# Optimization experiments

Hardware: AMD Instinct MI355X
Metric: run time of the kernel (lower is better)

## Reference

```python
import jax, jax.numpy as jnp
import numpy as np

BLOCK_SIZE = 128  # config.block_size; first query block skips intra-block causal mask (faithful to source)
NEG = -1e9       # the module uses -1e9, not -inf, for masking and m_i init


def setup_inputs() -> dict:
    key = jax.random.key(0)
    kq, kk, kv, km = jax.random.split(key, 4)
    B, S, H, D = 2, 2048, 16, 64
    q = jax.random.normal(kq, (B, S, H, D), dtype=jnp.float32)
    k = jax.random.normal(kk, (B, S, H, D), dtype=jnp.float32)
    v = jax.random.normal(kv, (B, S, H, D), dtype=jnp.float32)
    mask = jax.random.randint(km, (B, S), 0, 2).astype(bool)
    mask = mask.at[:, 0].set(True)  # keep first key attendable
    return {"q": q, "k": k, "v": v, "mask": mask}


def reference(q, k, v, mask):
    # q,k,v: [B,S,H,D]; mask: [B,S] bool (True = attend)
    B, S, H, D = q.shape
    scale = 1.0 / np.sqrt(D)
    # config.normalize_query=True -> F.normalize(q, dim=-1) (eps=1e-12)
    qn = q / jnp.maximum(jnp.linalg.norm(q, axis=-1, keepdims=True), 1e-12)
    # scores: [B,S(query),H,S(key)]
    scores = jnp.einsum('bshd,bkhd->bshk', qn, k) * scale
    qi = jnp.arange(S)[:, None]
    ki = jnp.arange(S)[None, :]
    # Faithful causal structure of the blocked PyTorch fallback:
    #  - keys limited to k <= q (triu(diagonal=block_start+1) masking)
    #  - EXCEPT the first query block (block_start==0), where the intra-block
    #    causal mask is skipped (keys still limited to the first block).
    allowed = (ki <= qi) | ((qi < BLOCK_SIZE) & (ki < BLOCK_SIZE))  # [S,S]
    scores = jnp.where(allowed[None, :, None, :], scores, NEG)
    scores = jnp.where(mask[:, None, None, :], scores, NEG)
    p = jax.nn.softmax(scores, axis=-1)
    out = jnp.einsum('bshk,bkhd->bshd', p, v)
    return out
```

## Files before the change

kernel.cpp:

```cpp
#include <hip/hip_runtime.h>
#include <stdint.h>

typedef __attribute__((ext_vector_type(8))) short short8;
typedef __attribute__((ext_vector_type(4))) float floatx4;
typedef __attribute__((ext_vector_type(4))) unsigned int uintx4;
typedef __attribute__((ext_vector_type(2))) unsigned int uintx2;
typedef unsigned long long ulong64;

#define S_LEN 2048
#define NHEAD 16
#define DHEAD 64
#define KB    64
#define KPL   131072
#define VPL   262144
#define VOFF  (32 * KPL)
#define MOFF  (VOFF + 32 * VPL)
#define POFF  (MOFF + 8192)
#define DOFF  (POFF + 512 * 32768)
#define WS_NEEDED ((size_t)DOFF + 512 * 512)
#define NEGINF (-__builtin_inff())
#define CSC   0.011271055f

static __device__ __forceinline__ unsigned f2bf(float f) {
    union { float f; unsigned u; } w; w.f = f;
    return (w.u + 0x7FFFu + ((w.u >> 16) & 1u)) >> 16;
}
static __device__ __forceinline__ unsigned cvtpk(float lo, float hi) {
    unsigned r;
    asm("v_cvt_pk_bf16_f32 %0, %1, %2" : "=v"(r) : "v"(lo), "v"(hi));
    return r;
}
template <int HI>
static __device__ __forceinline__ int cvtfp8(float a, float b, int old) {
    return __builtin_amdgcn_cvt_pk_fp8_f32(a, b, old, HI);
}
static __device__ __forceinline__ floatx4 mfma16(short8 a, short8 b, floatx4 c) {
    return __builtin_amdgcn_mfma_f32_16x16x32_bf16(a, b, c, 0, 0, 0);
}
static __device__ __forceinline__ floatx4 mfma8(long a, long b, floatx4 c) {
    return __builtin_amdgcn_mfma_f32_16x16x32_fp8_fp8(a, b, c, 0, 0, 0);
}

__global__ __launch_bounds__(256) void prep_kernel(
    const float* __restrict__ kg, const float* __restrict__ vg,
    const int* __restrict__ mg, char* __restrict__ ws)
{
    __shared__ unsigned short Tl[64 * 72];
    const int bid = blockIdx.x;
    const int t   = bid & 31;
    const int bh  = bid >> 5;
    const int b   = bh >> 4, h = bh & 15;
    const int tid = threadIdx.x;
    char* kpre = ws + (size_t)bh * KPL;
    char* vpre = ws + VOFF + (size_t)bh * VPL;

    #pragma unroll
    for (int r2 = 0; r2 < 2; ++r2) {
        const int ss  = tid + r2 * 256;
        const int khs = ss >> 8;
        const int mt  = (ss >> 7) & 1;
        const int ksd = (ss >> 6) & 1;
        const int ln  = ss & 63;
        const int key = khs * 32 + mt * 16 + (ln & 15);
        const int d0  = 32 * ksd + 8 * (ln >> 4);
        const float* kr = kg + (((size_t)b * S_LEN + t * 64 + key) * NHEAD + h) * DHEAD + d0;
        floatx4 f0 = *(const floatx4*)(kr);
        floatx4 f1 = *(const floatx4*)(kr + 4);
        int w0 = 0, w1 = 0;
        w0 = cvtfp8<0>(f0[0], f0[1], w0); w0 = cvtfp8<1>(f0[2], f0[3], w0);
        w1 = cvtfp8<0>(f1[0], f1[1], w1); w1 = cvtfp8<1>(f1[2], f1[3], w1);
        *(uintx2*)(kpre + t * 4096 + ss * 8) = (uintx2){(unsigned)w0, (unsigned)w1};
    }
    {
        const int key = tid >> 2;
        const int d0  = (tid & 3) * 16;
        const float vz = mg[(size_t)b * S_LEN + t * 64 + key] ? 1.f : 0.f;
        const size_t grow = (((size_t)b * S_LEN + t * 64 + key) * NHEAD + h) * DHEAD;
        #pragma unroll
        for (int q = 0; q < 4; ++q) {
            floatx4 f = *(const floatx4*)(vg + grow + d0 + 4 * q);
            #pragma unroll
            for (int ii = 0; ii < 4; ++ii)
                Tl[(d0 + 4 * q + ii) * 72 + key] = (unsigned short)f2bf(f[ii] * vz);
        }
    }
    __syncthreads();
    #pragma unroll
    for (int r2 = 0; r2 < 2; ++r2) {
        const int ss  = tid + r2 * 256;
        const int khs = ss >> 8;
        const int nt  = (ss >> 6) & 3;
        const int ln  = ss & 63;
        const int d   = 16 * nt + (ln & 15);
        const int pg  = 4 * khs + (ln >> 4);
        unsigned short vals[8];
        #pragma unroll
        for (int i = 0; i < 8; ++i) {
            const int p   = pg * 8 + i;
            const int blk = p >> 5;
            const int a   = (p >> 3) & 3;
            const int key = 32 * blk + ((i < 4) ? (4 * a + i) : (16 + 4 * a + i - 4));
            vals[i] = Tl[d * 72 + key];
        }
        *(uintx4*)(vpre + t * 8192 + ss * 16) = *(const uintx4*)vals;
    }
    if (h == 0 && tid < 64) {
        const int key = tid;
        const int gg = (key >> 2) & 3, lo = key & 3;
        const int ks = key >> 5,      hi = (key >> 4) & 1;
        const unsigned short mv = mg[(size_t)b * S_LEN + t * 64 + key] ? 0x3F80 : 0;
        *(unsigned short*)(ws + MOFF + (size_t)b * 4096 + t * 128
                           + gg * 32 + ks * 16 + (4 * hi + lo) * 2) = mv;
    }
}

__global__ __launch_bounds__(512, 4) void fa3_main(
    const float* __restrict__ qg, char* __restrict__ ws,
    float* __restrict__ og)
{
    __shared__ char smem[32768];
    char* Qs = smem;

    const int tid  = threadIdx.x;
    const int bid  = blockIdx.x;
    const int gidx = bid >> 5;
    const int bh   = bid & 31;
    int qb, chunk; bool split;
    if (gidx < 16) { qb = 15 - (gidx >> 1); chunk = gidx & 1; split = true; }
    else           { qb = 7 - (gidx - 16);  chunk = 0;        split = false; }
    const int b    = bh >> 4;
    const int h    = bh & 15;
    const int w    = tid >> 6;
    const int lane = tid & 63;
    const int g    = lane >> 4;
    const int lm   = lane & 15;
    const int kh   = w >> 2;
    const int wq   = w & 3;
    const int nkt = (qb == 0) ? 2 : (2 * qb + 2);
    int kt0 = 0, kt1 = nkt;
    if (split) { const int hh = nkt >> 1; kt0 = chunk ? hh : 0; kt1 = chunk ? nkt : hh; }

    {
        const int r  = tid >> 2;
        const int q0 = tid & 3;
        const float* src = qg + (((size_t)b * S_LEN + (size_t)qb * 128 + r) * NHEAD + h) * DHEAD + q0 * 16;
        floatx4 f0 = *(const floatx4*)(src + 0);
        floatx4 f1 = *(const floatx4*)(src + 4);
        floatx4 f2 = *(const floatx4*)(src + 8);
        floatx4 f3 = *(const floatx4*)(src + 12);
        float ssq = 0.f;
        #pragma unroll
        for (int i = 0; i < 4; ++i)
            ssq += f0[i]*f0[i] + f1[i]*f1[i] + f2[i]*f2[i] + f3[i]*f3[i];
        ssq += __shfl_xor(ssq, 1);
        ssq += __shfl_xor(ssq, 2);
        const float sc = 16.0f / fmaxf(sqrtf(ssq), 1e-12f);
        int w0 = 0, w1 = 0, w2 = 0, w3 = 0;
        w0 = cvtfp8<0>(f0[0]*sc, f0[1]*sc, w0); w0 = cvtfp8<1>(f0[2]*sc, f0[3]*sc, w0);
        w1 = cvtfp8<0>(f1[0]*sc, f1[1]*sc, w1); w1 = cvtfp8<1>(f1[2]*sc, f1[3]*sc, w1);
        w2 = cvtfp8<0>(f2[0]*sc, f2[1]*sc, w2); w2 = cvtfp8<1>(f2[2]*sc, f2[3]*sc, w2);
        w3 = cvtfp8<0>(f3[0]*sc, f3[1]*sc, w3); w3 = cvtfp8<1>(f3[2]*sc, f3[3]*sc, w3);
        const int Xr = r & 7;
        char* qp = Qs + r * 64 + 8 * (((2 * q0) ^ Xr) & ~1);
        *(uintx4*)qp = (Xr & 1)
            ? (uintx4){(unsigned)w2, (unsigned)w3, (unsigned)w0, (unsigned)w1}
            : (uintx4){(unsigned)w0, (unsigned)w1, (unsigned)w2, (unsigned)w3};
    }
    __syncthreads();

    const int Xl8 = (lm & 7) << 3;
    long qf8[2][2];
    #pragma unroll
    for (int grp = 0; grp < 2; ++grp) {
        const char* base = Qs + (wq * 32 + grp * 16 + lm) * 64;
        #pragma unroll
        for (int ksd = 0; ksd < 2; ++ksd)
            qf8[grp][ksd] = *(const long*)(base + ((32 * ksd + 8 * g) ^ Xl8));
    }

    const char* kp = ws + (size_t)bh * KPL + (size_t)kt0 * 4096 + kh * 2048 + lane * 8;
    const char* vp = ws + VOFF + (size_t)bh * VPL + (size_t)kt0 * 8192 + kh * 4096 + lane * 16;
    const char* mp = ws + MOFF + (size_t)b * 4096 + (size_t)kt0 * 128 + g * 32 + kh * 16;

    floatx4 oacc[2][4];
    floatx4 dacc[2];
    #pragma unroll
    for (int grp = 0; grp < 2; ++grp) {
        dacc[grp] = (floatx4){0.f,0.f,0.f,0.f};
        #pragma unroll
        for (int nt = 0; nt < 4; ++nt) oacc[grp][nt] = (floatx4){0.f,0.f,0.f,0.f};
    }
    floatx4 ZERO4 = (floatx4){0.f,0.f,0.f,0.f};
    asm volatile("" : "+v"(ZERO4));
    const int qgl0 = qb * 128 + wq * 32 + lm;

    for (int kt = kt0; kt < kt1; ++kt) {
        const ulong64 k00 = *(const ulong64*)(kp);
        const ulong64 k01 = *(const ulong64*)(kp + 512);
        const ulong64 k10 = *(const ulong64*)(kp + 1024);
        const ulong64 k11 = *(const ulong64*)(kp + 1536);
        const short8 vf0 = *(const short8*)(vp);
        const short8 vf1 = *(const short8*)(vp + 1024);
        const short8 vf2 = *(const short8*)(vp + 2048);
        const short8 vf3 = *(const short8*)(vp + 3072);
        const short8 mf  = *(const short8*)(mp);
        kp += 4096; vp += 8192; mp += 128;

        floatx4 st[2][2];
        __builtin_amdgcn_s_setprio(1);
        st[0][0] = mfma8((long)k00, qf8[0][0], ZERO4);
        st[1][0] = mfma8((long)k00, qf8[1][0], ZERO4);
        st[0][1] = mfma8((long)k10, qf8[0][0], ZERO4);
        st[1][1] = mfma8((long)k10, qf8[1][0], ZERO4);
        st[0][0] = mfma8((long)k01, qf8[0][1], st[0][0]);
        st[1][0] = mfma8((long)k01, qf8[1][1], st[1][0]);
        st[0][1] = mfma8((long)k11, qf8[0][1], st[0][1]);
        st[1][1] = mfma8((long)k11, qf8[1][1], st[1][1]);
        __builtin_amdgcn_s_setprio(0);

        if ((qb >= 1) && (kt >= 2 * qb)) {
            #pragma unroll
            for (int mt = 0; mt < 2; ++mt)
                #pragma unroll
                for (int j = 0; j < 4; ++j) {
                    const int kgl = kt * KB + kh * 32 + mt * 16 + 4 * g + j;
                    if (kgl > qgl0)      st[0][mt][j] = -1e6f;
                    if (kgl > qgl0 + 16) st[1][mt][j] = -1e6f;
                }
        }

        short8 pa[2];
        #pragma unroll
        for (int grp = 0; grp < 2; ++grp) {
            float p[8];
            #pragma unroll
            for (int mt = 0; mt < 2; ++mt)
                #pragma unroll
                for (int j = 0; j < 4; ++j)
                    p[mt * 4 + j] = exp2f(fmaf(st[grp][mt][j], CSC, -8.0f));
            union { short8 s; uintx4 u; } pu;
            pu.u = (uintx4){ cvtpk(p[0], p[1]), cvtpk(p[2], p[3]),
                             cvtpk(p[4], p[5]), cvtpk(p[6], p[7]) };
            pa[grp] = pu.s;
        }
        __builtin_amdgcn_s_setprio(1);
        dacc[0] = mfma16(pa[0], mf, dacc[0]);
        dacc[1] = mfma16(pa[1], mf, dacc[1]);
        oacc[0][0] = mfma16(pa[0], vf0, oacc[0][0]);
        oacc[1][0] = mfma16(pa[1], vf0, oacc[1][0]);
        oacc[0][1] = mfma16(pa[0], vf1, oacc[0][1]);
        oacc[1][1] = mfma16(pa[1], vf1, oacc[1][1]);
        oacc[0][2] = mfma16(pa[0], vf2, oacc[0][2]);
        oacc[1][2] = mfma16(pa[1], vf2, oacc[1][2]);
        oacc[0][3] = mfma16(pa[0], vf3, oacc[0][3]);
        oacc[1][3] = mfma16(pa[1], vf3, oacc[1][3]);
        __builtin_amdgcn_s_setprio(0);
    }
    __syncthreads();

    floatx4* rbuf = (floatx4*)smem;
    float*   dbuf = (float*)smem;
    if (kh == 1) {
        #pragma unroll
        for (int grp = 0; grp < 2; ++grp)
            #pragma unroll
            for (int nt = 0; nt < 4; ++nt)
                rbuf[((grp * 4 + nt) * 4 + wq) * 64 + lane] = oacc[grp][nt];
    }
    __syncthreads();
    if (kh == 0) {
        #pragma unroll
        for (int grp = 0; grp < 2; ++grp)
            #pragma unroll
            for (int nt = 0; nt < 4; ++nt)
                oacc[grp][nt] += rbuf[((grp * 4 + nt) * 4 + wq) * 64 + lane];
    }
    __syncthreads();
    if (kh == 1 && lm == 0) {
        #pragma unroll
        for (int grp = 0; grp < 2; ++grp)
            #pragma unroll
            for (int j = 0; j < 4; ++j)
                dbuf[wq * 32 + grp * 16 + 4 * g + j] = dacc[grp][j];
    }
    __syncthreads();
    if (kh == 0) {
        if (!split) {
            #pragma unroll
            for (int grp = 0; grp < 2; ++grp)
                #pragma unroll
                for (int j = 0; j < 4; ++j) {
                    const int rl = wq * 32 + grp * 16 + 4 * g + j;
                    const float invj = 1.0f / (dacc[grp][j] + dbuf[rl]);
                    float* dst = og + (((size_t)b * S_LEN + qb * 128 + rl) * NHEAD + h) * DHEAD + lm;
                    #pragma unroll
                    for (int nt = 0; nt < 4; ++nt) dst[nt * 16] = oacc[grp][nt][j] * invj;
                }
        } else {
            const int s = ((qb - 8) * 32 + bh) * 2 + chunk;
            float* po = (float*)(ws + POFF + (size_t)s * 32768);
            float* pd = (float*)(ws + DOFF + (size_t)s * 512);
            #pragma unroll
            for (int grp = 0; grp < 2; ++grp)
                #pragma unroll
                for (int j = 0; j < 4; ++j) {
                    const int rl = wq * 32 + grp * 16 + 4 * g + j;
                    #pragma unroll
                    for (int nt = 0; nt < 4; ++nt)
                        po[rl * 64 + nt * 16 + lm] = oacc[grp][nt][j];
                    if (lm == 0) pd[rl] = dacc[grp][j] + dbuf[rl];
                }
        }
    }
}

__global__ __launch_bounds__(256) void fa3_combine(
    const char* __restrict__ ws, float* __restrict__ og)
{
    const int i0  = (blockIdx.x * 256 + threadIdx.x) * 8;
    const int d   = i0 & 63;
    const int row = (i0 >> 6) & 127;
    const int bh  = (i0 >> 13) & 31;
    const int qbi = i0 >> 18;
    const int b   = bh >> 4, h = bh & 15;
    const int s0  = (qbi * 32 + bh) * 2;
    const float* p0 = (const float*)(ws + POFF + (size_t)s0 * 32768) + row * 64 + d;
    const float* p1 = (const float*)(ws + POFF + (size_t)(s0 + 1) * 32768) + row * 64 + d;
    const float den = ((const float*)(ws + DOFF + (size_t)s0 * 512))[row]
                    + ((const float*)(ws + DOFF + (size_t)(s0 + 1) * 512))[row];
    const float inv = 1.0f / den;
    floatx4 a0 = *(const floatx4*)p0, a1 = *(const floatx4*)(p0 + 4);
    floatx4 b0 = *(const floatx4*)p1, b1 = *(const floatx4*)(p1 + 4);
    floatx4 o0, o1;
    #pragma unroll
    for (int i = 0; i < 4; ++i) { o0[i] = (a0[i] + b0[i]) * inv; o1[i] = (a1[i] + b1[i]) * inv; }
    float* dst = og + (((size_t)b * S_LEN + (8 + qbi) * 128 + row) * NHEAD + h) * DHEAD + d;
    *(floatx4*)dst       = o0;
    *(floatx4*)(dst + 4) = o1;
}

__global__ __launch_bounds__(512) void fa3_fallback(
    const float* __restrict__ qg, const float* __restrict__ kg,
    const float* __restrict__ vg, const int* __restrict__ mg,
    float* __restrict__ og)
{
    __shared__ unsigned short Qs[128 * DHEAD];
    __shared__ unsigned short Ks2[KB * DHEAD];
    __shared__ unsigned short Vt[DHEAD * KB];
    __shared__ float Ms[KB];

    const int tid  = threadIdx.x;
    const int bid  = blockIdx.x;
    const int qb   = 15 - (bid >> 5);
    const int bh   = bid & 31;
    const int b    = bh >> 4;
    const int h    = bh & 15;
    const int w    = tid >> 6;
    const int lane = tid & 63;
    const int g    = lane >> 4;
    const int lm   = lane & 15;

    {
        const int r  = tid >> 2;
        const int q0 = tid & 3;
        const float* src = qg + (((size_t)b * S_LEN + (size_t)qb * 128 + r) * NHEAD + h) * DHEAD + q0 * 16;
        floatx4 f0 = *(const floatx4*)(src + 0);
        floatx4 f1 = *(const floatx4*)(src + 4);
        floatx4 f2 = *(const floatx4*)(src + 8);
        floatx4 f3 = *(const floatx4*)(src + 12);
        float ssq = 0.f;
        #pragma unroll
        for (int i = 0; i < 4; ++i)
            ssq += f0[i]*f0[i] + f1[i]*f1[i] + f2[i]*f2[i] + f3[i]*f3[i];
        ssq += __shfl_xor(ssq, 1);
        ssq += __shfl_xor(ssq, 2);
        const float sc = 0.125f / fmaxf(sqrtf(ssq), 1e-12f);
        float fv[16];
        #pragma unroll
        for (int i = 0; i < 4; ++i) { fv[i]=f0[i]; fv[4+i]=f1[i]; fv[8+i]=f2[i]; fv[12+i]=f3[i]; }
        unsigned pk[8];
        #pragma unroll
        for (int i = 0; i < 8; ++i)
            pk[i] = f2bf(fv[2*i]*sc) | (f2bf(fv[2*i+1]*sc) << 16);
        const int X = (r & 7) << 4;
        char* qp = (char*)Qs + r * 128;
        *(uintx4*)(qp + ((32*q0)      ^ X)) = (uintx4){pk[0],pk[1],pk[2],pk[3]};
        *(uintx4*)(qp + ((32*q0 + 16) ^ X)) = (uintx4){pk[4],pk[5],pk[6],pk[7]};
    }
    __syncthreads();

    short8 qf[2];
    {
        const int row = w * 16 + lm;
        const int X = (row & 7) << 4;
        const char* base = (const char*)Qs + row * 128;
        #pragma unroll
        for (int ks = 0; ks < 2; ++ks) {
            union { short8 s; uintx2 u[2]; } u;
            u.u[0] = *(const uintx2*)(base + ((64*ks + 8*g)      ^ X));
            u.u[1] = *(const uintx2*)(base + ((64*ks + 8*g + 32) ^ X));
            qf[ks] = u.s;
        }
    }

    floatx4 oacc[4];
    #pragma unroll
    for (int nt = 0; nt < 4; ++nt) oacc[nt] = (floatx4){0.f,0.f,0.f,0.f};
    float mrun = NEGINF, lrun = 0.f;
    const int q_glob = qb * 128 + w * 16 + lm;
    const int nkt = (qb == 0) ? 2 : (2 * qb + 2);

    for (int kt = 0; kt < nkt; ++kt) {
        const int kb0 = kt * KB;
        {
            const int r = tid >> 3;
            const int o = tid & 7;
            const size_t goff = (((size_t)b * S_LEN + kb0 + r) * NHEAD + h) * DHEAD + o * 8;
            floatx4 a0 = *(const floatx4*)(kg + goff);
            floatx4 a1 = *(const floatx4*)(kg + goff + 4);
            floatx4 c0 = *(const floatx4*)(vg + goff);
            floatx4 c1 = *(const floatx4*)(vg + goff + 4);
            uintx4 kw = (uintx4){ f2bf(a0[0]) | (f2bf(a0[1])<<16),
                                  f2bf(a0[2]) | (f2bf(a0[3])<<16),
                                  f2bf(a1[0]) | (f2bf(a1[1])<<16),
                                  f2bf(a1[2]) | (f2bf(a1[3])<<16) };
            *(uintx4*)((char*)Ks2 + r*128 + ((16*o) ^ ((r & 7) << 4))) = kw;
            float cv[8];
            #pragma unroll
            for (int i = 0; i < 4; ++i) { cv[i] = c0[i]; cv[4+i] = c1[i]; }
            #pragma unroll
            for (int i = 0; i < 8; ++i) {
                const int d = 8*o + i;
                Vt[d*64 + (r ^ (((i ^ o) & 7) << 3))] = (unsigned short)f2bf(cv[i]);
            }
            if (tid < KB) Ms[tid] = mg[(size_t)b * S_LEN + kb0 + tid] ? 0.f : NEGINF;
        }
        __syncthreads();

        floatx4 st[4];
        #pragma unroll
        for (int mt = 0; mt < 4; ++mt) st[mt] = (floatx4){0.f,0.f,0.f,0.f};
        #pragma unroll
        for (int ks = 0; ks < 2; ++ks) {
            #pragma unroll
            for (int mt = 0; mt < 4; ++mt) {
                const int row = mt * 16 + lm;
                const int X = (row & 7) << 4;
                const char* base = (const char*)Ks2 + row * 128;
                union { short8 s; uintx2 u[2]; } u;
                u.u[0] = *(const uintx2*)(base + ((64*ks + 8*g)      ^ X));
                u.u[1] = *(const uintx2*)(base + ((64*ks + 8*g + 32) ^ X));
                st[mt] = mfma16(u.s, qf[ks], st[mt]);
            }
        }

        const bool diag = (qb > 0) && (kt >= 2 * qb);
        float sv[16];
        #pragma unroll
        for (int mt = 0; mt < 4; ++mt) {
            #pragma unroll
            for (int j = 0; j < 4; ++j) {
                const int kl = mt * 16 + 4 * g + j;
                float s = st[mt][j] + Ms[kl];
                if (diag && (kb0 + kl > q_glob)) s = NEGINF;
                sv[mt * 4 + j] = s;
            }
        }

        float rmax = sv[0];
        #pragma unroll
        for (int i = 1; i < 16; ++i) rmax = fmaxf(rmax, sv[i]);
        rmax = fmaxf(rmax, __shfl_xor(rmax, 16));
        rmax = fmaxf(rmax, __shfl_xor(rmax, 32));
        const float mnew = fmaxf(mrun, rmax);
        const float cf = __expf(mrun - mnew);
        float p[16], psum = 0.f;
        #pragma unroll
        for (int i = 0; i < 16; ++i) { p[i] = __expf(sv[i] - mnew); psum += p[i]; }
        psum += __shfl_xor(psum, 16);
        psum += __shfl_xor(psum, 32);
        lrun = lrun * cf + psum;
        mrun = mnew;

        float cj[4];
        #pragma unroll
        for (int j = 0; j < 4; ++j) cj[j] = __shfl(cf, 20 * g + j);
        #pragma unroll
        for (int nt = 0; nt < 4; ++nt)
            #pragma unroll
            for (int j = 0; j < 4; ++j) oacc[nt][j] *= cj[j];

        short8 pa[2];
        #pragma unroll
        for (int ks = 0; ks < 2; ++ks)
            #pragma unroll
            for (int i = 0; i < 8; ++i)
                pa[ks][i] = (short)f2bf(p[(2*ks + (i>>2))*4 + (i&3)]);

        #pragma unroll
        for (int nt = 0; nt < 4; ++nt) {
            const int d = 16 * nt + lm;
            const int xz = (((d & 7) ^ ((d >> 3) & 7)) & 7) << 4;
            const char* vb = (const char*)Vt + d * 128;
            #pragma unroll
            for (int ks = 0; ks < 2; ++ks) {
                union { short8 s; uintx2 u[2]; } vu;
                vu.u[0] = *(const uintx2*)(vb + ((64*ks + 8*g)      ^ xz));
                vu.u[1] = *(const uintx2*)(vb + ((64*ks + 8*g + 32) ^ xz));
                oacc[nt] = mfma16(pa[ks], vu.s, oacc[nt]);
            }
        }
        __syncthreads();
    }

    const float inv = 1.0f / lrun;
    #pragma unroll
    for (int j = 0; j < 4; ++j) {
        const float invj = __shfl(inv, 20 * g + j);
        const int row = qb * 128 + w * 16 + 4 * g + j;
        float* dst = og + (((size_t)b * S_LEN + row) * NHEAD + h) * DHEAD + lm;
        #pragma unroll
        for (int nt = 0; nt < 4; ++nt) dst[nt * 16] = oacc[nt][j] * invj;
    }
}

extern "C" void kernel_launch(void* const* d_in, const int* in_sizes, int n_in,
                              void* d_out, int out_size, void* d_ws, size_t ws_size,
                              hipStream_t stream)
{
    const float* q = (const float*)d_in[0];
    const float* k = (const float*)d_in[1];
    const float* v = (const float*)d_in[2];
    const int*   m = (const int*)d_in[3];
    float* out = (float*)d_out;
    (void)in_sizes; (void)n_in; (void)out_size;
    if (ws_size >= WS_NEEDED) {
        prep_kernel<<<dim3(1024), dim3(256), 0, stream>>>(k, v, m, (char*)d_ws);
        fa3_main<<<dim3(768), dim3(512), 0, stream>>>(q, (char*)d_ws, out);
        fa3_combine<<<dim3(1024), dim3(256), 0, stream>>>((const char*)d_ws, out);
    } else {
        fa3_fallback<<<dim3(512), dim3(512), 0, stream>>>(q, k, v, m, out);
    }
}
```

Before: 52.88 us.

## Widen K prepack to 16-byte loads and double-buffer K tiles in main loop

The prep kernel now packs K so each lane stores and later reads 16 contiguous bytes, which turns four 8-byte K loads per tile into two 16-byte loads. The main loop is unrolled by two, with explicit register double-buffering that loads the next tile's K while the current tile computes. The non-split query blocks are also reordered to ascending qb. This spends more registers to hide global load latency and cut load instruction count, which may hurt occupancy under launch_bounds(512,4).

```diff
diff --git a/kernel.cpp b/kernel.cpp
--- a/kernel.cpp
+++ b/kernel.cpp
@@ -5,7 +5,6 @@
 typedef __attribute__((ext_vector_type(4))) float floatx4;
 typedef __attribute__((ext_vector_type(4))) unsigned int uintx4;
 typedef __attribute__((ext_vector_type(2))) unsigned int uintx2;
-typedef unsigned long long ulong64;
 
 #define S_LEN 2048
 #define NHEAD 16
@@ -54,22 +53,25 @@
     char* kpre = ws + (size_t)bh * KPL;
     char* vpre = ws + VOFF + (size_t)bh * VPL;
 
-    #pragma unroll
-    for (int r2 = 0; r2 < 2; ++r2) {
-        const int ss  = tid + r2 * 256;
-        const int khs = ss >> 8;
-        const int mt  = (ss >> 7) & 1;
-        const int ksd = (ss >> 6) & 1;
-        const int ln  = ss & 63;
-        const int key = khs * 32 + mt * 16 + (ln & 15);
-        const int d0  = 32 * ksd + 8 * (ln >> 4);
-        const float* kr = kg + (((size_t)b * S_LEN + t * 64 + key) * NHEAD + h) * DHEAD + d0;
-        floatx4 f0 = *(const floatx4*)(kr);
-        floatx4 f1 = *(const floatx4*)(kr + 4);
-        int w0 = 0, w1 = 0;
+    {
+        const int khs = tid >> 7;
+        const int ksd = (tid >> 6) & 1;
+        const int ln  = tid & 63;
+        const int key0 = khs * 32 + (ln & 15);
+        const int d0   = 32 * ksd + 8 * (ln >> 4);
+        const float* r0 = kg + (((size_t)b * S_LEN + t * 64 + key0) * NHEAD + h) * DHEAD + d0;
+        const float* r1 = r0 + 16 * NHEAD * DHEAD;
+        floatx4 f0 = *(const floatx4*)(r0);
+        floatx4 f1 = *(const floatx4*)(r0 + 4);
+        floatx4 f2 = *(const floatx4*)(r1);
+        floatx4 f3 = *(const floatx4*)(r1 + 4);
+        int w0 = 0, w1 = 0, w2 = 0, w3 = 0;
         w0 = cvtfp8<0>(f0[0], f0[1], w0); w0 = cvtfp8<1>(f0[2], f0[3], w0);
         w1 = cvtfp8<0>(f1[0], f1[1], w1); w1 = cvtfp8<1>(f1[2], f1[3], w1);
-        *(uintx2*)(kpre + t * 4096 + ss * 8) = (uintx2){(unsigned)w0, (unsigned)w1};
+        w2 = cvtfp8<0>(f2[0], f2[1], w2); w2 = cvtfp8<1>(f2[2], f2[3], w2);
+        w3 = cvtfp8<0>(f3[0], f3[1], w3); w3 = cvtfp8<1>(f3[2], f3[3], w3);
+        *(uintx4*)(kpre + t * 4096 + tid * 16) =
+            (uintx4){(unsigned)w0, (unsigned)w1, (unsigned)w2, (unsigned)w3};
     }
     {
         const int key = tid >> 2;
@@ -127,7 +129,7 @@
     const int bh   = bid & 31;
     int qb, chunk; bool split;
     if (gidx < 16) { qb = 15 - (gidx >> 1); chunk = gidx & 1; split = true; }
-    else           { qb = 7 - (gidx - 16);  chunk = 0;        split = false; }
+    else           { qb = gidx - 16;        chunk = 0;        split = false; }
     const int b    = bh >> 4;
     const int h    = bh & 15;
     const int w    = tid >> 6;
@@ -178,9 +180,9 @@
             qf8[grp][ksd] = *(const long*)(base + ((32 * ksd + 8 * g) ^ Xl8));
     }
 
-    const char* kp = ws + (size_t)bh * KPL + (size_t)kt0 * 4096 + kh * 2048 + lane * 8;
-    const char* vp = ws + VOFF + (size_t)bh * VPL + (size_t)kt0 * 8192 + kh * 4096 + lane * 16;
-    const char* mp = ws + MOFF + (size_t)b * 4096 + (size_t)kt0 * 128 + g * 32 + kh * 16;
+    const char* kpb = ws + (size_t)bh * KPL + kh * 2048 + lane * 16;
+    const char* vpb = ws + VOFF + (size_t)bh * VPL + kh * 4096 + lane * 16;
+    const char* mpb = ws + MOFF + (size_t)b * 4096 + g * 32 + kh * 16;
 
     floatx4 oacc[2][4];
     floatx4 dacc[2];
@@ -194,68 +196,91 @@
     asm volatile("" : "+v"(ZERO4));
     const int qgl0 = qb * 128 + wq * 32 + lm;
 
-    for (int kt = kt0; kt < kt1; ++kt) {
-        const ulong64 k00 = *(const ulong64*)(kp);
-        const ulong64 k01 = *(const ulong64*)(kp + 512);
-        const ulong64 k10 = *(const ulong64*)(kp + 1024);
-        const ulong64 k11 = *(const ulong64*)(kp + 1536);
-        const short8 vf0 = *(const short8*)(vp);
-        const short8 vf1 = *(const short8*)(vp + 1024);
-        const short8 vf2 = *(const short8*)(vp + 2048);
-        const short8 vf3 = *(const short8*)(vp + 3072);
-        const short8 mf  = *(const short8*)(mp);
-        kp += 4096; vp += 8192; mp += 128;
-
-        floatx4 st[2][2];
-        __builtin_amdgcn_s_setprio(1);
-        st[0][0] = mfma8((long)k00, qf8[0][0], ZERO4);
-        st[1][0] = mfma8((long)k00, qf8[1][0], ZERO4);
-        st[0][1] = mfma8((long)k10, qf8[0][0], ZERO4);
-        st[1][1] = mfma8((long)k10, qf8[1][0], ZERO4);
-        st[0][0] = mfma8((long)k01, qf8[0][1], st[0][0]);
-        st[1][0] = mfma8((long)k01, qf8[1][1], st[1][0]);
-        st[0][1] = mfma8((long)k11, qf8[0][1], st[0][1]);
-        st[1][1] = mfma8((long)k11, qf8[1][1], st[1][1]);
-        __builtin_amdgcn_s_setprio(0);
-
-        if ((qb >= 1) && (kt >= 2 * qb)) {
-            #pragma unroll
-            for (int mt = 0; mt < 2; ++mt)
-                #pragma unroll
-                for (int j = 0; j < 4; ++j) {
-                    const int kgl = kt * KB + kh * 32 + mt * 16 + 4 * g + j;
-                    if (kgl > qgl0)      st[0][mt][j] = -1e6f;
-                    if (kgl > qgl0 + 16) st[1][mt][j] = -1e6f;
-                }
-        }
-
-        short8 pa[2];
-        #pragma unroll
-        for (int grp = 0; grp < 2; ++grp) {
-            float p[8];
-            #pragma unroll
-            for (int mt = 0; mt < 2; ++mt)
-                #pragma unroll
-                for (int j = 0; j < 4; ++j)
-                    p[mt * 4 + j] = exp2f(fmaf(st[grp][mt][j], CSC, -8.0f));
-            union { short8 s; uintx4 u; } pu;
-            pu.u = (uintx4){ cvtpk(p[0], p[1]), cvtpk(p[2], p[3]),
-                             cvtpk(p[4], p[5]), cvtpk(p[6], p[7]) };
-            pa[grp] = pu.s;
-        }
-        __builtin_amdgcn_s_setprio(1);
-        dacc[0] = mfma16(pa[0], mf, dacc[0]);
-        dacc[1] = mfma16(pa[1], mf, dacc[1]);
-        oacc[0][0] = mfma16(pa[0], vf0, oacc[0][0]);
-        oacc[1][0] = mfma16(pa[1], vf0, oacc[1][0]);
-        oacc[0][1] = mfma16(pa[0], vf1, oacc[0][1]);
-        oacc[1][1] = mfma16(pa[1], vf1, oacc[1][1]);
-        oacc[0][2] = mfma16(pa[0], vf2, oacc[0][2]);
-        oacc[1][2] = mfma16(pa[1], vf2, oacc[1][2]);
-        oacc[0][3] = mfma16(pa[0], vf3, oacc[0][3]);
-        oacc[1][3] = mfma16(pa[1], vf3, oacc[1][3]);
-        __builtin_amdgcn_s_setprio(0);
-    }
+#define LOAD_K(K0V, K1V, KT) do {                                          \
+        const char* kpt_ = kpb + (size_t)(KT) * 4096;                      \
+        (K0V) = *(const uintx4*)(kpt_);                                    \
+        (K1V) = *(const uintx4*)(kpt_ + 1024);                             \
+    } while (0)
+
+#define COMPUTE_TILE(KT, K0V, K1V) do {                                    \
+        const char* vpt_ = vpb + (size_t)(KT) * 8192;                      \
+        const short8 vf0_ = *(const short8*)(vpt_);                        \
+        const short8 vf1_ = *(const short8*)(vpt_ + 1024);                 \
+        const short8 vf2_ = *(const short8*)(vpt_ + 2048);                 \
+        const short8 vf3_ = *(const short8*)(vpt_ + 3072);                 \
+        const short8 mf_  = *(const short8*)(mpb + (size_t)(KT) * 128);    \
+        union { uintx4 u; long l[2]; } ua_, ub_;                           \
+        ua_.u = (K0V); ub_.u = (K1V);                                      \
+        floatx4 st00, st01, st10, st11;                                    \
+        __builtin_amdgcn_s_setprio(1);                                     \
+        st00 = mfma8(ua_.l[0], qf8[0][0], ZERO4);                          \
+        st10 = mfma8(ua_.l[0], qf8[1][0], ZERO4);                          \
+        st01 = mfma8(ua_.l[1], qf8[0][0], ZERO4);                          \
+        st11 = mfma8(ua_.l[1], qf8[1][0], ZERO4);                          \
+        st00 = mfma8(ub_.l[0], qf8[0][1], st00);                           \
+        st10 = mfma8(ub_.l[0], qf8[1][1], st10);                           \
+        st01 = mfma8(ub_.l[1], qf8[0][1], st01);                           \
+        st11 = mfma8(ub_.l[1], qf8[1][1], st11);                           \
+        __builtin_amdgcn_s_setprio(0);                                     \
+        if ((qb >= 1) && ((KT) >= 2 * qb)) {                               \
+            _Pragma("unroll")                                              \
+            for (int j = 0; j < 4; ++j) {                                  \
+                const int kg0 = (KT) * KB + kh * 32 + 4 * g + j;           \
+                if (kg0 > qgl0)           st00[j] = -1e6f;                 \
+                if (kg0 + 16 > qgl0)      st01[j] = -1e6f;                 \
+                if (kg0 > qgl0 + 16)      st10[j] = -1e6f;                 \
+                if (kg0 + 16 > qgl0 + 16) st11[j] = -1e6f;                 \
+            }                                                              \
+        }                                                                  \
+        short8 pa0_, pa1_;                                                 \
+        {                                                                  \
+            float p[8];                                                    \
+            _Pragma("unroll")                                              \
+            for (int j = 0; j < 4; ++j) {                                  \
+                p[j]     = exp2f(fmaf(st00[j], CSC, -8.0f));               \
+                p[4 + j] = exp2f(fmaf(st01[j], CSC, -8.0f));               \
+            }                                                              \
+            union { short8 s; uintx4 u; } pu_;                             \
+            pu_.u = (uintx4){ cvtpk(p[0], p[1]), cvtpk(p[2], p[3]),        \
+                              cvtpk(p[4], p[5]), cvtpk(p[6], p[7]) };      \
+            pa0_ = pu_.s;                                                  \
+            _Pragma("unroll")                                              \
+            for (int j = 0; j < 4; ++j) {                                  \
+                p[j]     = exp2f(fmaf(st10[j], CSC, -8.0f));               \
+                p[4 + j] = exp2f(fmaf(st11[j], CSC, -8.0f));               \
+            }                                                              \
+            pu_.u = (uintx4){ cvtpk(p[0], p[1]), cvtpk(p[2], p[3]),        \
+                              cvtpk(p[4], p[5]), cvtpk(p[6], p[7]) };      \
+            pa1_ = pu_.s;                                                  \
+        }                                                                  \
+        __builtin_amdgcn_s_setprio(1);                                     \
+        dacc[0] = mfma16(pa0_, mf_, dacc[0]);                              \
+        dacc[1] = mfma16(pa1_, mf_, dacc[1]);                              \
+        oacc[0][0] = mfma16(pa0_, vf0_, oacc[0][0]);                       \
+        oacc[1][0] = mfma16(pa1_, vf0_, oacc[1][0]);                       \
+        oacc[0][1] = mfma16(pa0_, vf1_, oacc[0][1]);                       \
+        oacc[1][1] = mfma16(pa1_, vf1_, oacc[1][1]);                       \
+        oacc[0][2] = mfma16(pa0_, vf2_, oacc[0][2]);                       \
+        oacc[1][2] = mfma16(pa1_, vf2_, oacc[1][2]);                       \
+        oacc[0][3] = mfma16(pa0_, vf3_, oacc[0][3]);                       \
+        oacc[1][3] = mfma16(pa1_, vf3_, oacc[1][3]);                       \
+        __builtin_amdgcn_s_setprio(0);                                     \
+    } while (0)
+
+    uintx4 k0A, k1A, k0B, k1B;
+    LOAD_K(k0A, k1A, kt0);
+    int kt = kt0;
+    while (kt + 2 <= kt1) {
+        LOAD_K(k0B, k1B, kt + 1);
+        COMPUTE_TILE(kt, k0A, k1A);
+        if (kt + 2 < kt1) LOAD_K(k0A, k1A, kt + 2);
+        COMPUTE_TILE(kt + 1, k0B, k1B);
+        kt += 2;
+    }
+    if (kt < kt1) COMPUTE_TILE(kt, k0A, k1A);
+#undef LOAD_K
+#undef COMPUTE_TILE
+
     __syncthreads();
 
     floatx4* rbuf = (floatx4*)smem;
```

Result: slower. 56.01 us (+5.9%).

## Replace in-block key-half split with finer split-K across blocks and 4-wave CTAs

Applied to the files above, without the earlier changes.

The main attention kernel no longer splits each key tile between two wave halves that reduce through shared memory. Each 256-thread block now processes full 64-key tiles per wave and query blocks 4..15 are split across 2-4 key-range chunks using lookup tables. This gives 1280 blocks and removes the intra-block LDS reduction and barriers. The K prep layout is changed to match 16-byte loads, and the combine kernel now sums a variable number of partials. The trade-off is more partial writes and reads through global workspace and a larger workspace requirement.

```diff
diff --git a/kernel.cpp b/kernel.cpp
--- a/kernel.cpp
+++ b/kernel.cpp
@@ -5,7 +5,6 @@
 typedef __attribute__((ext_vector_type(4))) float floatx4;
 typedef __attribute__((ext_vector_type(4))) unsigned int uintx4;
 typedef __attribute__((ext_vector_type(2))) unsigned int uintx2;
-typedef unsigned long long ulong64;
 
 #define S_LEN 2048
 #define NHEAD 16
@@ -16,10 +15,17 @@
 #define VOFF  (32 * KPL)
 #define MOFF  (VOFF + 32 * VPL)
 #define POFF  (MOFF + 8192)
-#define DOFF  (POFF + 512 * 32768)
-#define WS_NEEDED ((size_t)DOFF + 512 * 512)
+#define DOFF  (POFF + (size_t)2048 * 32768)
+#define WS_NEEDED ((size_t)DOFF + 2048 * 512)
 #define NEGINF (-__builtin_inff())
 #define CSC   0.011271055f
+
+__device__ const unsigned char QBT[40] = {15,15,15,15,14,14,14,14,13,13,13,13,
+                                          12,12,12,12,11,11,11,10,10,10,9,9,9,
+                                          8,8,8,7,7,6,6,5,5,4,4,3,2,1,0};
+__device__ const unsigned char CIT[40] = {0,1,2,3,0,1,2,3,0,1,2,3,0,1,2,3,
+                                          0,1,2,0,1,2,0,1,2,0,1,2,0,1,0,1,
+                                          0,1,0,1,0,0,0,0};
 
 static __device__ __forceinline__ unsigned f2bf(float f) {
     union { float f; unsigned u; } w; w.f = f;
@@ -54,22 +60,25 @@
     char* kpre = ws + (size_t)bh * KPL;
     char* vpre = ws + VOFF + (size_t)bh * VPL;
 
-    #pragma unroll
-    for (int r2 = 0; r2 < 2; ++r2) {
-        const int ss  = tid + r2 * 256;
-        const int khs = ss >> 8;
-        const int mt  = (ss >> 7) & 1;
-        const int ksd = (ss >> 6) & 1;
-        const int ln  = ss & 63;
-        const int key = khs * 32 + mt * 16 + (ln & 15);
-        const int d0  = 32 * ksd + 8 * (ln >> 4);
-        const float* kr = kg + (((size_t)b * S_LEN + t * 64 + key) * NHEAD + h) * DHEAD + d0;
-        floatx4 f0 = *(const floatx4*)(kr);
-        floatx4 f1 = *(const floatx4*)(kr + 4);
-        int w0 = 0, w1 = 0;
+    {
+        const int pr = tid >> 6;
+        const int ln = tid & 63;
+        const int a  = pr >> 1, c = pr & 1;
+        const int keyA = a * 16 + (ln & 15);
+        const int d0   = 32 * c + 8 * (ln >> 4);
+        const float* r0 = kg + (((size_t)b * S_LEN + t * 64 + keyA) * NHEAD + h) * DHEAD + d0;
+        const float* r1 = r0 + 32 * NHEAD * DHEAD;
+        floatx4 f0 = *(const floatx4*)(r0);
+        floatx4 f1 = *(const floatx4*)(r0 + 4);
+        floatx4 f2 = *(const floatx4*)(r1);
+        floatx4 f3 = *(const floatx4*)(r1 + 4);
+        int w0 = 0, w1 = 0, w2 = 0, w3 = 0;
         w0 = cvtfp8<0>(f0[0], f0[1], w0); w0 = cvtfp8<1>(f0[2], f0[3], w0);
         w1 = cvtfp8<0>(f1[0], f1[1], w1); w1 = cvtfp8<1>(f1[2], f1[3], w1);
-        *(uintx2*)(kpre + t * 4096 + ss * 8) = (uintx2){(unsigned)w0, (unsigned)w1};
+        w2 = cvtfp8<0>(f2[0], f2[1], w2); w2 = cvtfp8<1>(f2[2], f2[3], w2);
+        w3 = cvtfp8<0>(f3[0], f3[1], w3); w3 = cvtfp8<1>(f3[2], f3[3], w3);
+        *(uintx4*)(kpre + t * 4096 + tid * 16) =
+            (uintx4){(unsigned)w0, (unsigned)w1, (unsigned)w2, (unsigned)w3};
     }
     {
         const int key = tid >> 2;
@@ -88,11 +97,11 @@
     #pragma unroll
     for (int r2 = 0; r2 < 2; ++r2) {
         const int ss  = tid + r2 * 256;
-        const int khs = ss >> 8;
+        const int hfs = ss >> 8;
         const int nt  = (ss >> 6) & 3;
         const int ln  = ss & 63;
         const int d   = 16 * nt + (ln & 15);
-        const int pg  = 4 * khs + (ln >> 4);
+        const int pg  = 4 * hfs + (ln >> 4);
         unsigned short vals[8];
         #pragma unroll
         for (int i = 0; i < 8; ++i) {
@@ -114,34 +123,38 @@
     }
 }
 
-__global__ __launch_bounds__(512, 4) void fa3_main(
+__global__ __launch_bounds__(256, 4) void fa3_main(
     const float* __restrict__ qg, char* __restrict__ ws,
     float* __restrict__ og)
 {
-    __shared__ char smem[32768];
+    __shared__ char smem[8192];
     char* Qs = smem;
 
     const int tid  = threadIdx.x;
     const int bid  = blockIdx.x;
     const int gidx = bid >> 5;
     const int bh   = bid & 31;
-    int qb, chunk; bool split;
-    if (gidx < 16) { qb = 15 - (gidx >> 1); chunk = gidx & 1; split = true; }
-    else           { qb = 7 - (gidx - 16);  chunk = 0;        split = false; }
+    const int qb   = QBT[gidx];
+    const int ci   = CIT[gidx];
     const int b    = bh >> 4;
     const int h    = bh & 15;
     const int w    = tid >> 6;
     const int lane = tid & 63;
     const int g    = lane >> 4;
     const int lm   = lane & 15;
-    const int kh   = w >> 2;
-    const int wq   = w & 3;
-    const int nkt = (qb == 0) ? 2 : (2 * qb + 2);
+    const int nkt  = (qb == 0) ? 2 : (2 * qb + 2);
+    const bool split = (qb >= 4);
     int kt0 = 0, kt1 = nkt;
-    if (split) { const int hh = nkt >> 1; kt0 = chunk ? hh : 0; kt1 = chunk ? nkt : hh; }
-
-    {
-        const int r  = tid >> 2;
+    if (split) {
+        const int c = (nkt + 7) >> 3;
+        const int base = nkt / c, rem = nkt % c;
+        kt0 = ci * base + (ci < rem ? ci : rem);
+        kt1 = kt0 + base + (ci < rem ? 1 : 0);
+    }
+
+    #pragma unroll
+    for (int rr = 0; rr < 2; ++rr) {
+        const int r  = rr * 64 + (tid >> 2);
         const int q0 = tid & 3;
         const float* src = qg + (((size_t)b * S_LEN + (size_t)qb * 128 + r) * NHEAD + h) * DHEAD + q0 * 16;
         floatx4 f0 = *(const floatx4*)(src + 0);
@@ -172,15 +185,15 @@
     long qf8[2][2];
     #pragma unroll
     for (int grp = 0; grp < 2; ++grp) {
-        const char* base = Qs + (wq * 32 + grp * 16 + lm) * 64;
+        const char* base = Qs + (w * 32 + grp * 16 + lm) * 64;
         #pragma unroll
         for (int ksd = 0; ksd < 2; ++ksd)
             qf8[grp][ksd] = *(const long*)(base + ((32 * ksd + 8 * g) ^ Xl8));
     }
 
-    const char* kp = ws + (size_t)bh * KPL + (size_t)kt0 * 4096 + kh * 2048 + lane * 8;
-    const char* vp = ws + VOFF + (size_t)bh * VPL + (size_t)kt0 * 8192 + kh * 4096 + lane * 16;
-    const char* mp = ws + MOFF + (size_t)b * 4096 + (size_t)kt0 * 128 + g * 32 + kh * 16;
+    const char* kpb = ws + (size_t)bh * KPL + lane * 16;
+    const char* vpb = ws + VOFF + (size_t)bh * VPL + lane * 16;
+    const char* mpb = ws + MOFF + (size_t)b * 4096 + g * 32;
 
     floatx4 oacc[2][4];
     floatx4 dacc[2];
@@ -192,125 +205,116 @@
     }
     floatx4 ZERO4 = (floatx4){0.f,0.f,0.f,0.f};
     asm volatile("" : "+v"(ZERO4));
-    const int qgl0 = qb * 128 + wq * 32 + lm;
+    const int qgl0 = qb * 128 + w * 32 + lm;
 
     for (int kt = kt0; kt < kt1; ++kt) {
-        const ulong64 k00 = *(const ulong64*)(kp);
-        const ulong64 k01 = *(const ulong64*)(kp + 512);
-        const ulong64 k10 = *(const ulong64*)(kp + 1024);
-        const ulong64 k11 = *(const ulong64*)(kp + 1536);
-        const short8 vf0 = *(const short8*)(vp);
-        const short8 vf1 = *(const short8*)(vp + 1024);
-        const short8 vf2 = *(const short8*)(vp + 2048);
-        const short8 vf3 = *(const short8*)(vp + 3072);
-        const short8 mf  = *(const short8*)(mp);
-        kp += 4096; vp += 8192; mp += 128;
-
-        floatx4 st[2][2];
+        const char* kpt = kpb + (size_t)kt * 4096;
+        union { uintx4 u; long l[2]; } kq0, kq1, kq2, kq3;
+        kq0.u = *(const uintx4*)(kpt);
+        kq1.u = *(const uintx4*)(kpt + 1024);
+        kq2.u = *(const uintx4*)(kpt + 2048);
+        kq3.u = *(const uintx4*)(kpt + 3072);
+        const char* vpt = vpb + (size_t)kt * 8192;
+        const short8 mf0 = *(const short8*)(mpb + (size_t)kt * 128);
+        const short8 mf1 = *(const short8*)(mpb + (size_t)kt * 128 + 16);
+
+        floatx4 st[2][4];
         __builtin_amdgcn_s_setprio(1);
-        st[0][0] = mfma8((long)k00, qf8[0][0], ZERO4);
-        st[1][0] = mfma8((long)k00, qf8[1][0], ZERO4);
-        st[0][1] = mfma8((long)k10, qf8[0][0], ZERO4);
-        st[1][1] = mfma8((long)k10, qf8[1][0], ZERO4);
-        st[0][0] = mfma8((long)k01, qf8[0][1], st[0][0]);
-        st[1][0] = mfma8((long)k01, qf8[1][1], st[1][0]);
-        st[0][1] = mfma8((long)k11, qf8[0][1], st[0][1]);
-        st[1][1] = mfma8((long)k11, qf8[1][1], st[1][1]);
+        #pragma unroll
+        for (int grp = 0; grp < 2; ++grp) {
+            st[grp][0] = mfma8(kq0.l[0], qf8[grp][0], ZERO4);
+            st[grp][2] = mfma8(kq0.l[1], qf8[grp][0], ZERO4);
+            st[grp][1] = mfma8(kq2.l[0], qf8[grp][0], ZERO4);
+            st[grp][3] = mfma8(kq2.l[1], qf8[grp][0], ZERO4);
+            st[grp][0] = mfma8(kq1.l[0], qf8[grp][1], st[grp][0]);
+            st[grp][2] = mfma8(kq1.l[1], qf8[grp][1], st[grp][2]);
+            st[grp][1] = mfma8(kq3.l[0], qf8[grp][1], st[grp][1]);
+            st[grp][3] = mfma8(kq3.l[1], qf8[grp][1], st[grp][3]);
+        }
         __builtin_amdgcn_s_setprio(0);
 
+        short8 vf00 = *(const short8*)(vpt);
+        short8 vf01 = *(const short8*)(vpt + 1024);
+        short8 vf02 = *(const short8*)(vpt + 2048);
+        short8 vf03 = *(const short8*)(vpt + 3072);
+        short8 vf10 = *(const short8*)(vpt + 4096);
+        short8 vf11 = *(const short8*)(vpt + 5120);
+        short8 vf12 = *(const short8*)(vpt + 6144);
+        short8 vf13 = *(const short8*)(vpt + 7168);
+
         if ((qb >= 1) && (kt >= 2 * qb)) {
             #pragma unroll
-            for (int mt = 0; mt < 2; ++mt)
+            for (int grp = 0; grp < 2; ++grp) {
+                const int qgl = qgl0 + grp * 16;
                 #pragma unroll
-                for (int j = 0; j < 4; ++j) {
-                    const int kgl = kt * KB + kh * 32 + mt * 16 + 4 * g + j;
-                    if (kgl > qgl0)      st[0][mt][j] = -1e6f;
-                    if (kgl > qgl0 + 16) st[1][mt][j] = -1e6f;
-                }
-        }
-
-        short8 pa[2];
+                for (int mt = 0; mt < 4; ++mt)
+                    #pragma unroll
+                    for (int j = 0; j < 4; ++j) {
+                        const int kgl = kt * KB + mt * 16 + 4 * g + j;
+                        if (kgl > qgl) st[grp][mt][j] = -1e6f;
+                    }
+            }
+        }
+
+        short8 pa[2][2];
         #pragma unroll
         for (int grp = 0; grp < 2; ++grp) {
-            float p[8];
-            #pragma unroll
-            for (int mt = 0; mt < 2; ++mt)
+            float p[16];
+            #pragma unroll
+            for (int mt = 0; mt < 4; ++mt)
                 #pragma unroll
                 for (int j = 0; j < 4; ++j)
                     p[mt * 4 + j] = exp2f(fmaf(st[grp][mt][j], CSC, -8.0f));
             union { short8 s; uintx4 u; } pu;
-            pu.u = (uintx4){ cvtpk(p[0], p[1]), cvtpk(p[2], p[3]),
-                             cvtpk(p[4], p[5]), cvtpk(p[6], p[7]) };
-            pa[grp] = pu.s;
+            #pragma unroll
+            for (int hf = 0; hf < 2; ++hf) {
+                pu.u = (uintx4){ cvtpk(p[8*hf+0], p[8*hf+1]), cvtpk(p[8*hf+2], p[8*hf+3]),
+                                 cvtpk(p[8*hf+4], p[8*hf+5]), cvtpk(p[8*hf+6], p[8*hf+7]) };
+                pa[grp][hf] = pu.s;
+            }
         }
         __builtin_amdgcn_s_setprio(1);
-        dacc[0] = mfma16(pa[0], mf, dacc[0]);
-        dacc[1] = mfma16(pa[1], mf, dacc[1]);
-        oacc[0][0] = mfma16(pa[0], vf0, oacc[0][0]);
-        oacc[1][0] = mfma16(pa[1], vf0, oacc[1][0]);
-        oacc[0][1] = mfma16(pa[0], vf1, oacc[0][1]);
-        oacc[1][1] = mfma16(pa[1], vf1, oacc[1][1]);
-        oacc[0][2] = mfma16(pa[0], vf2, oacc[0][2]);
-        oacc[1][2] = mfma16(pa[1], vf2, oacc[1][2]);
-        oacc[0][3] = mfma16(pa[0], vf3, oacc[0][3]);
-        oacc[1][3] = mfma16(pa[1], vf3, oacc[1][3]);
+        #pragma unroll
+        for (int grp = 0; grp < 2; ++grp) {
+            dacc[grp] = mfma16(pa[grp][0], mf0, dacc[grp]);
+            dacc[grp] = mfma16(pa[grp][1], mf1, dacc[grp]);
+            oacc[grp][0] = mfma16(pa[grp][0], vf00, oacc[grp][0]);
+            oacc[grp][1] = mfma16(pa[grp][0], vf01, oacc[grp][1]);
+            oacc[grp][2] = mfma16(pa[grp][0], vf02, oacc[grp][2]);
+            oacc[grp][3] = mfma16(pa[grp][0], vf03, oacc[grp][3]);
+            oacc[grp][0] = mfma16(pa[grp][1], vf10, oacc[grp][0]);
+            oacc[grp][1] = mfma16(pa[grp][1], vf11, oacc[grp][1]);
+            oacc[grp][2] = mfma16(pa[grp][1], vf12, oacc[grp][2]);
+            oacc[grp][3] = mfma16(pa[grp][1], vf13, oacc[grp][3]);
+        }
         __builtin_amdgcn_s_setprio(0);
     }
-    __syncthreads();
-
-    floatx4* rbuf = (floatx4*)smem;
-    float*   dbuf = (float*)smem;
-    if (kh == 1) {
+
+    if (!split) {
         #pragma unroll
         for (int grp = 0; grp < 2; ++grp)
             #pragma unroll
-            for (int nt = 0; nt < 4; ++nt)
-                rbuf[((grp * 4 + nt) * 4 + wq) * 64 + lane] = oacc[grp][nt];
-    }
-    __syncthreads();
-    if (kh == 0) {
+            for (int j = 0; j < 4; ++j) {
+                const int rl = w * 32 + grp * 16 + 4 * g + j;
+                const float invj = 1.0f / dacc[grp][j];
+                float* dst = og + (((size_t)b * S_LEN + qb * 128 + rl) * NHEAD + h) * DHEAD + lm;
+                #pragma unroll
+                for (int nt = 0; nt < 4; ++nt) dst[nt * 16] = oacc[grp][nt][j] * invj;
+            }
+    } else {
+        const int s = (qb * 4 + ci) * 32 + bh;
+        float* po = (float*)(ws + POFF + (size_t)s * 32768);
+        float* pd = (float*)(ws + DOFF + (size_t)s * 512);
         #pragma unroll
         for (int grp = 0; grp < 2; ++grp)
             #pragma unroll
-            for (int nt = 0; nt < 4; ++nt)
-                oacc[grp][nt] += rbuf[((grp * 4 + nt) * 4 + wq) * 64 + lane];
-    }
-    __syncthreads();
-    if (kh == 1 && lm == 0) {
-        #pragma unroll
-        for (int grp = 0; grp < 2; ++grp)
-            #pragma unroll
-            for (int j = 0; j < 4; ++j)
-                dbuf[wq * 32 + grp * 16 + 4 * g + j] = dacc[grp][j];
-    }
-    __syncthreads();
-    if (kh == 0) {
-        if (!split) {
-            #pragma unroll
-            for (int grp = 0; grp < 2; ++grp)
+            for (int j = 0; j < 4; ++j) {
+                const int rl = w * 32 + grp * 16 + 4 * g + j;
                 #pragma unroll
-                for (int j = 0; j < 4; ++j) {
-                    const int rl = wq * 32 + grp * 16 + 4 * g + j;
-                    const float invj = 1.0f / (dacc[grp][j] + dbuf[rl]);
-                    float* dst = og + (((size_t)b * S_LEN + qb * 128 + rl) * NHEAD + h) * DHEAD + lm;
-                    #pragma unroll
-                    for (int nt = 0; nt < 4; ++nt) dst[nt * 16] = oacc[grp][nt][j] * invj;
-                }
-        } else {
-            const int s = ((qb - 8) * 32 + bh) * 2 + chunk;
-            float* po = (float*)(ws + POFF + (size_t)s * 32768);
-            float* pd = (float*)(ws + DOFF + (size_t)s * 512);
-            #pragma unroll
-            for (int grp = 0; grp < 2; ++grp)
-                #pragma unroll
-                for (int j = 0; j < 4; ++j) {
-                    const int rl = wq * 32 + grp * 16 + 4 * g + j;
-                    #pragma unroll
-                    for (int nt = 0; nt < 4; ++nt)
-                        po[rl * 64 + nt * 16 + lm] = oacc[grp][nt][j];
-                    if (lm == 0) pd[rl] = dacc[grp][j] + dbuf[rl];
-                }
-        }
+                for (int nt = 0; nt < 4; ++nt)
+                    po[rl * 64 + nt * 16 + lm] = oacc[grp][nt][j];
+                if (lm == 0) pd[rl] = dacc[grp][j];
+            }
     }
 }
 
@@ -322,19 +326,24 @@
     const int row = (i0 >> 6) & 127;
     const int bh  = (i0 >> 13) & 31;
     const int qbi = i0 >> 18;
+    const int qb  = 4 + qbi;
     const int b   = bh >> 4, h = bh & 15;
-    const int s0  = (qbi * 32 + bh) * 2;
-    const float* p0 = (const float*)(ws + POFF + (size_t)s0 * 32768) + row * 64 + d;
-    const float* p1 = (const float*)(ws + POFF + (size_t)(s0 + 1) * 32768) + row * 64 + d;
-    const float den = ((const float*)(ws + DOFF + (size_t)s0 * 512))[row]
-                    + ((const float*)(ws + DOFF + (size_t)(s0 + 1) * 512))[row];
+    const int nch = (qb >= 12) ? 4 : (qb >= 8) ? 3 : 2;
+    const int s0  = qb * 4 * 32 + bh;
+    floatx4 o0 = (floatx4){0.f,0.f,0.f,0.f}, o1 = (floatx4){0.f,0.f,0.f,0.f};
+    float den = 0.f;
+    for (int ci = 0; ci < nch; ++ci) {
+        const int s = s0 + ci * 32;
+        const float* po = (const float*)(ws + POFF + (size_t)s * 32768) + row * 64 + d;
+        floatx4 a0 = *(const floatx4*)po, a1 = *(const floatx4*)(po + 4);
+        #pragma unroll
+        for (int i = 0; i < 4; ++i) { o0[i] += a0[i]; o1[i] += a1[i]; }
+        den += ((const float*)(ws + DOFF + (size_t)s * 512))[row];
+    }
     const float inv = 1.0f / den;
-    floatx4 a0 = *(const floatx4*)p0, a1 = *(const floatx4*)(p0 + 4);
-    floatx4 b0 = *(const floatx4*)p1, b1 = *(const floatx4*)(p1 + 4);
-    floatx4 o0, o1;
-    #pragma unroll
-    for (int i = 0; i < 4; ++i) { o0[i] = (a0[i] + b0[i]) * inv; o1[i] = (a1[i] + b1[i]) * inv; }
-    float* dst = og + (((size_t)b * S_LEN + (8 + qbi) * 128 + row) * NHEAD + h) * DHEAD + d;
+    #pragma unroll
+    for (int i = 0; i < 4; ++i) { o0[i] *= inv; o1[i] *= inv; }
+    float* dst = og + (((size_t)b * S_LEN + qb * 128 + row) * NHEAD + h) * DHEAD + d;
     *(floatx4*)dst       = o0;
     *(floatx4*)(dst + 4) = o1;
 }
@@ -536,8 +545,8 @@
     (void)in_sizes; (void)n_in; (void)out_size;
     if (ws_size >= WS_NEEDED) {
         prep_kernel<<<dim3(1024), dim3(256), 0, stream>>>(k, v, m, (char*)d_ws);
-        fa3_main<<<dim3(768), dim3(512), 0, stream>>>(q, (char*)d_ws, out);
-        fa3_combine<<<dim3(1024), dim3(256), 0, stream>>>((const char*)d_ws, out);
+        fa3_main<<<dim3(1280), dim3(256), 0, stream>>>(q, (char*)d_ws, out);
+        fa3_combine<<<dim3(1536), dim3(256), 0, stream>>>((const char*)d_ws, out);
     } else {
         fa3_fallback<<<dim3(512), dim3(512), 0, stream>>>(q, k, v, m, out);
     }
```

New measurement: 105.8 us. +100.1%, slower.
